# Optimization experiments

Hardware: AMD Instinct MI355X
Metric: run time of the kernel (lower is better)

The kernel has to match this reference:

```python
import jax, jax.numpy as jnp
import numpy as np

VOCAB = 50000
EMBED = 512
COMP = 300
B, L = 2048, 200
CENTER = jnp.array([40.7127, -74.0059], dtype=jnp.float32)


def setup_inputs() -> dict:
    key = jax.random.key(0)
    ks = jax.random.split(key, 8)
    words = jax.random.randint(ks[0], (B, L), 0, VOCAB, dtype=jnp.int64)
    features = jax.random.normal(ks[1], (B, 2), dtype=jnp.float32)
    mask = jnp.ones((B, L), dtype=jnp.float32)
    # nn.Linear(vocab_size, embedding_dim): weight [out, in]
    lim1 = 1.0 / np.sqrt(VOCAB)
    W_hidden = jax.random.uniform(ks[2], (EMBED, VOCAB), jnp.float32, -lim1, lim1)
    b_hidden = jax.random.uniform(ks[3], (EMBED,), jnp.float32, -lim1, lim1)
    lim2 = 1.0 / np.sqrt(EMBED)
    W_pi = jax.random.uniform(ks[4], (COMP, EMBED), jnp.float32, -lim2, lim2)
    b_pi = jax.random.uniform(ks[5], (COMP,), jnp.float32, -lim2, lim2)
    # mu = (rand-0.5)*4 + CENTER ; sigma = rand * log(0.01)
    mu = (jax.random.uniform(ks[6], (COMP, 2), jnp.float32) - 0.5) * 4.0 + CENTER
    sigma = jax.random.uniform(ks[7], (COMP, 2), jnp.float32) * np.log(0.01).astype(np.float32)
    return {"words": words, "features": features, "mask": mask,
            "W_hidden": W_hidden, "b_hidden": b_hidden,
            "W_pi": W_pi, "b_pi": b_pi, "mu": mu, "sigma": sigma}


def reference(words, features, mask, W_hidden, b_hidden, W_pi, b_pi, mu, sigma):
    bsz = words.shape[0]
    # binary bag-of-words one-hot: s[words[i]] = 1 (duplicates collapse to 1)
    q = jnp.zeros((bsz, VOCAB), dtype=W_hidden.dtype)
    q = q.at[jnp.arange(bsz)[:, None], words].set(1.0)
    hidden = jnp.tanh(q @ W_hidden.T + b_hidden)          # [B, E]
    pi = jax.nn.softmax(hidden @ W_pi.T + b_pi, axis=-1).T  # [C, B]
    sigma_out = jnp.exp(sigma)                             # [C, 2]
    return pi, sigma_out, mu
```

## Files before the change

kernel.cpp:

```cpp
#include <hip/hip_runtime.h>
#include <cstdint>
#include <cstddef>

#define VOCAB 50000
#define EMBED 512
#define COMP  300
#define LW    200
#define LPAD  208
#define NCHUNK 8
#define CHUNK_ROWS 50048
#define CHUNK_BYTES ((size_t)CHUNK_ROWS * 64)
#define CPAD  320

#define QINVSCALE 28398.0633f
#define QSCALE    3.52136689e-05f

__global__ __launch_bounds__(256) void quant_chunk_kernel(
    const float* __restrict__ in, unsigned char* __restrict__ out)
{
    __shared__ float tile[64 * 68];
    const int wBase = blockIdx.x * 64;
    const int c = blockIdx.y;
    const int eBase = c * 64;
    const int t = threadIdx.x;

    {
        const int col4 = t & 15;
        const int w = wBase + col4 * 4;
#pragma unroll
        for (int rr = 0; rr < 4; ++rr) {
            const int el = (t >> 4) + rr * 16;
            float4 v = make_float4(0.f, 0.f, 0.f, 0.f);
            if (w + 3 < VOCAB) {
                v = *(const float4*)&in[(size_t)(eBase + el) * VOCAB + w];
            } else {
                const float* row = &in[(size_t)(eBase + el) * VOCAB];
                v.x = (w + 0 < VOCAB) ? row[w + 0] : 0.f;
                v.y = (w + 1 < VOCAB) ? row[w + 1] : 0.f;
                v.z = (w + 2 < VOCAB) ? row[w + 2] : 0.f;
                v.w = (w + 3 < VOCAB) ? row[w + 3] : 0.f;
            }
            *(float4*)&tile[el * 68 + col4 * 4] = v;
        }
    }
    __syncthreads();

    {
        const int wl = t >> 2;
        const int g = t & 3;
        unsigned int pk[4];
#pragma unroll
        for (int q4 = 0; q4 < 4; ++q4) {
            unsigned int p = 0;
#pragma unroll
            for (int k = 0; k < 4; ++k) {
                const float f = tile[(g * 16 + q4 * 4 + k) * 68 + wl];
                int q = __float2int_rn(f * QINVSCALE) + 128;
                q = q < 0 ? 0 : (q > 255 ? 255 : q);
                p |= (unsigned int)q << (8 * k);
            }
            pk[q4] = p;
        }
        uint4 v = make_uint4(pk[0], pk[1], pk[2], pk[3]);
        *(uint4*)(out + (size_t)c * CHUNK_BYTES + (size_t)(wBase + wl) * 64 + g * 16) = v;
    }
}

__global__ __launch_bounds__(512) void wpi_tail_kernel(
    const float* __restrict__ W_pi, const float* __restrict__ mu,
    const float* __restrict__ sigma, float* __restrict__ Wtp,
    float* __restrict__ out_tail)
{
    const int c = blockIdx.x;
    const int k = threadIdx.x;
    Wtp[(size_t)k * CPAD + c] = (c < COMP) ? W_pi[(size_t)c * EMBED + k] : 0.f;
    if (c == 0) {
        for (int t = k; t < 2 * COMP; t += 512) {
            out_tail[t]            = expf(sigma[t]);
            out_tail[2 * COMP + t] = mu[t];
        }
    }
}

__global__ __launch_bounds__(256) void dedup_kernel(
    const int* __restrict__ words, int* __restrict__ soff)
{
    __shared__ int sw[LW];
    const int i = blockIdx.x;
    const int t = threadIdx.x;
    if (t < LW) sw[t] = words[(size_t)i * LW + t];
    __syncthreads();
    if (t < LPAD) {
        int off = VOCAB * 64;
        if (t < LW) {
            const int w = sw[t];
            int dup = 0;
            for (int j = 0; j < t; ++j) dup |= (sw[j] == w);
            off = (dup ? VOCAB : w) * 64;
        }
        soff[(size_t)i * LPAD + t] = off;
    }
}

__global__ __launch_bounds__(256) void gather_kernel(
    const int* __restrict__ soff, const unsigned char* __restrict__ W8,
    const float* __restrict__ b_hidden, float* __restrict__ hT, int B)
{
    __shared__ int sOff[LPAD];
    __shared__ float part[256];
    const int b = blockIdx.x;
    const int c = b & 7;
    const int i = b >> 3;
    const int t = threadIdx.x;
    const int w4 = t >> 6, lane = t & 63;

    if (t < LPAD) sOff[t] = soff[(size_t)i * LPAD + t];
    __syncthreads();

    const unsigned char* base = W8 + (size_t)c * CHUNK_BYTES + (lane & 15) * 4;
    const int j = lane >> 4;
    const int l0 = w4 * 52;
    float a0 = 0.f, a1 = 0.f, a2 = 0.f, a3 = 0.f;
#pragma unroll
    for (int s = 0; s < 13; ++s) {
        const int off = sOff[l0 + s * 4 + j];
        const unsigned int d = *(const unsigned int*)(base + (unsigned int)off);
        a0 += (float)(d & 0xffu);
        a1 += (float)((d >> 8) & 0xffu);
        a2 += (float)((d >> 16) & 0xffu);
        a3 += (float)(d >> 24);
    }
    a0 += __shfl_xor(a0, 16); a0 += __shfl_xor(a0, 32);
    a1 += __shfl_xor(a1, 16); a1 += __shfl_xor(a1, 32);
    a2 += __shfl_xor(a2, 16); a2 += __shfl_xor(a2, 32);
    a3 += __shfl_xor(a3, 16); a3 += __shfl_xor(a3, 32);
    if (lane < 16)
        *(float4*)&part[w4 * 64 + lane * 4] = make_float4(a0, a1, a2, a3);
    __syncthreads();

    if (t < 64) {
        const float S = part[t] + part[64 + t] + part[128 + t] + part[192 + t];
        const int e = c * 64 + t;
        hT[(size_t)e * B + i] = tanhf((S - 26624.0f) * QSCALE + b_hidden[e]);
    }
}

__global__ __launch_bounds__(256) void logits_kernel(
    const float* __restrict__ hT, const float* __restrict__ Wtp,
    const float* __restrict__ b_pi, float* __restrict__ logit, int B)
{
    __shared__ float sh[256 * 64];
    const int i0 = blockIdx.x * 64;
    const int cblk = blockIdx.y;
    const int t = threadIdx.x;
    const int wv = __builtin_amdgcn_readfirstlane(t >> 6);
    const int lane = t & 63;
    const int c0 = cblk * 32 + wv * 8;

    float acc[8] = {0.f, 0.f, 0.f, 0.f, 0.f, 0.f, 0.f, 0.f};

    for (int ks = 0; ks < EMBED; ks += 256) {
        __syncthreads();
#pragma unroll
        for (int p = 0; p < 16; ++p) {
            const int q = p * 256 + t;
            const int k = q >> 4;
            const int f4 = q & 15;
            *(float4*)&sh[k * 64 + f4 * 4] =
                *(const float4*)&hT[(size_t)(ks + k) * B + i0 + f4 * 4];
        }
        __syncthreads();

#pragma unroll 4
        for (int k = 0; k < 256; ++k) {
            const float h = sh[k * 64 + lane];
            const float* __restrict__ wrow = &Wtp[(size_t)(ks + k) * CPAD + c0];
#pragma unroll
            for (int jj = 0; jj < 8; ++jj)
                acc[jj] = fmaf(h, wrow[jj], acc[jj]);
        }
    }

#pragma unroll
    for (int jj = 0; jj < 8; ++jj) {
        const int cc = c0 + jj;
        if (cc < COMP)
            logit[(size_t)cc * B + i0 + lane] = acc[jj] + b_pi[cc];
    }
}

__global__ __launch_bounds__(64) void softmax_kernel(
    const float* __restrict__ logit, float* __restrict__ pi_out, int B)
{
    const int i = blockIdx.x * 64 + threadIdx.x;
    float m = -INFINITY, l = 0.f;
#pragma unroll 4
    for (int c = 0; c < COMP; ++c) {
        const float x = logit[(size_t)c * B + i];
        const float mn = fmaxf(m, x);
        l = l * __expf(m - mn) + __expf(x - mn);
        m = mn;
    }
    const float inv = 1.0f / l;
#pragma unroll 4
    for (int c = 0; c < COMP; ++c) {
        const float x = logit[(size_t)c * B + i];
        pi_out[(size_t)c * B + i] = __expf(x - m) * inv;
    }
}

extern "C" void kernel_launch(void* const* d_in, const int* in_sizes, int n_in,
                              void* d_out, int out_size, void* d_ws, size_t ws_size,
                              hipStream_t stream) {
    const int*   words    = (const int*)d_in[0];
    const float* W_hidden = (const float*)d_in[3];
    const float* b_hidden = (const float*)d_in[4];
    const float* W_pi     = (const float*)d_in[5];
    const float* b_pi     = (const float*)d_in[6];
    const float* mu       = (const float*)d_in[7];
    const float* sigma    = (const float*)d_in[8];
    float* out = (float*)d_out;

    const int B = in_sizes[0] / LW;

    unsigned char* W8   = (unsigned char*)d_ws;
    int*   soff  = (int*)(W8 + NCHUNK * CHUNK_BYTES);
    float* hT    = (float*)(soff + (size_t)B * LPAD);
    float* Wtp   = hT + (size_t)EMBED * B;
    float* logit = Wtp + (size_t)EMBED * CPAD;

    hipLaunchKernelGGL(quant_chunk_kernel, dim3(CHUNK_ROWS / 64, NCHUNK), dim3(256),
                       0, stream, W_hidden, W8);
    hipLaunchKernelGGL(wpi_tail_kernel, dim3(CPAD), dim3(512), 0, stream,
                       W_pi, mu, sigma, Wtp, out + (size_t)COMP * B);
    hipLaunchKernelGGL(dedup_kernel, dim3(B), dim3(256), 0, stream, words, soff);
    hipLaunchKernelGGL(gather_kernel, dim3(B * NCHUNK), dim3(256), 0, stream,
                       soff, W8, b_hidden, hT, B);
    hipLaunchKernelGGL(logits_kernel, dim3(B / 64, 10), dim3(256), 0, stream,
                       hT, Wtp, b_pi, logit, B);
    hipLaunchKernelGGL(softmax_kernel, dim3(B / 64), dim3(64), 0, stream,
                       logit, out, B);
}
```

Before: 290.6 us.

## Coalesce hidden and W_pi transposes, split softmax with partial max/sum

```diff
diff --git a/kernel.cpp b/kernel.cpp
--- a/kernel.cpp
+++ b/kernel.cpp
@@ -11,6 +11,7 @@
 #define CHUNK_ROWS 50048
 #define CHUNK_BYTES ((size_t)CHUNK_ROWS * 64)
 #define CPAD  320
+#define NPART 40
 
 #define QINVSCALE 28398.0633f
 #define QSCALE    3.52136689e-05f
@@ -66,18 +67,42 @@
     }
 }
 
-__global__ __launch_bounds__(512) void wpi_tail_kernel(
+__global__ __launch_bounds__(256) void wpi_tail_kernel(
     const float* __restrict__ W_pi, const float* __restrict__ mu,
     const float* __restrict__ sigma, float* __restrict__ Wtp,
     float* __restrict__ out_tail)
 {
-    const int c = blockIdx.x;
-    const int k = threadIdx.x;
-    Wtp[(size_t)k * CPAD + c] = (c < COMP) ? W_pi[(size_t)c * EMBED + k] : 0.f;
-    if (c == 0) {
-        for (int t = k; t < 2 * COMP; t += 512) {
-            out_tail[t]            = expf(sigma[t]);
-            out_tail[2 * COMP + t] = mu[t];
+    __shared__ float tile[32 * 33];
+    const int kBase = blockIdx.x * 32;
+    const int cBase = blockIdx.y * 32;
+    const int t = threadIdx.x;
+
+    {
+        const int cr = t >> 3;
+        const int k4 = t & 7;
+        float4 v = make_float4(0.f, 0.f, 0.f, 0.f);
+        if (cBase + cr < COMP)
+            v = *(const float4*)&W_pi[(size_t)(cBase + cr) * EMBED + kBase + k4 * 4];
+        tile[cr * 33 + k4 * 4 + 0] = v.x;
+        tile[cr * 33 + k4 * 4 + 1] = v.y;
+        tile[cr * 33 + k4 * 4 + 2] = v.z;
+        tile[cr * 33 + k4 * 4 + 3] = v.w;
+    }
+    __syncthreads();
+    {
+        const int kr = t >> 3;
+        const int c4 = t & 7;
+        float4 v;
+        v.x = tile[(c4 * 4 + 0) * 33 + kr];
+        v.y = tile[(c4 * 4 + 1) * 33 + kr];
+        v.z = tile[(c4 * 4 + 2) * 33 + kr];
+        v.w = tile[(c4 * 4 + 3) * 33 + kr];
+        *(float4*)&Wtp[(size_t)(kBase + kr) * CPAD + cBase + c4 * 4] = v;
+    }
+    if (blockIdx.x == 0 && blockIdx.y == 0) {
+        for (int tt = t; tt < 2 * COMP; tt += 256) {
+            out_tail[tt]            = expf(sigma[tt]);
+            out_tail[2 * COMP + tt] = mu[tt];
         }
     }
 }
@@ -104,7 +129,7 @@
 
 __global__ __launch_bounds__(256) void gather_kernel(
     const int* __restrict__ soff, const unsigned char* __restrict__ W8,
-    const float* __restrict__ b_hidden, float* __restrict__ hT, int B)
+    const float* __restrict__ b_hidden, float* __restrict__ h)
 {
     __shared__ int sOff[LPAD];
     __shared__ float part[256];
@@ -141,15 +166,48 @@
     if (t < 64) {
         const float S = part[t] + part[64 + t] + part[128 + t] + part[192 + t];
         const int e = c * 64 + t;
-        hT[(size_t)e * B + i] = tanhf((S - 26624.0f) * QSCALE + b_hidden[e]);
+        h[(size_t)i * EMBED + e] = tanhf((S - 26624.0f) * QSCALE + b_hidden[e]);
+    }
+}
+
+__global__ __launch_bounds__(256) void htrans_kernel(
+    const float* __restrict__ h, float* __restrict__ hT, int B)
+{
+    __shared__ float tile[64 * 65];
+    const int i0 = blockIdx.x * 64;
+    const int k0 = blockIdx.y * 64;
+    const int t = threadIdx.x;
+    const int col4 = t & 15;
+    const int row = t >> 4;
+
+#pragma unroll
+    for (int rr = 0; rr < 4; ++rr) {
+        const int r = row + rr * 16;
+        const float4 v = *(const float4*)&h[(size_t)(i0 + r) * EMBED + k0 + col4 * 4];
+        tile[r * 65 + col4 * 4 + 0] = v.x;
+        tile[r * 65 + col4 * 4 + 1] = v.y;
+        tile[r * 65 + col4 * 4 + 2] = v.z;
+        tile[r * 65 + col4 * 4 + 3] = v.w;
+    }
+    __syncthreads();
+#pragma unroll
+    for (int rr = 0; rr < 4; ++rr) {
+        const int kr = row + rr * 16;
+        float4 v;
+        v.x = tile[(col4 * 4 + 0) * 65 + kr];
+        v.y = tile[(col4 * 4 + 1) * 65 + kr];
+        v.z = tile[(col4 * 4 + 2) * 65 + kr];
+        v.w = tile[(col4 * 4 + 3) * 65 + kr];
+        *(float4*)&hT[(size_t)(k0 + kr) * B + i0 + col4 * 4] = v;
     }
 }
 
 __global__ __launch_bounds__(256) void logits_kernel(
     const float* __restrict__ hT, const float* __restrict__ Wtp,
-    const float* __restrict__ b_pi, float* __restrict__ logit, int B)
-{
-    __shared__ float sh[256 * 64];
+    const float* __restrict__ b_pi, float* __restrict__ logit,
+    float* __restrict__ pm, float* __restrict__ pl, int B)
+{
+    __shared__ float sh[128 * 64];
     const int i0 = blockIdx.x * 64;
     const int cblk = blockIdx.y;
     const int t = threadIdx.x;
@@ -159,10 +217,10 @@
 
     float acc[8] = {0.f, 0.f, 0.f, 0.f, 0.f, 0.f, 0.f, 0.f};
 
-    for (int ks = 0; ks < EMBED; ks += 256) {
+    for (int ks = 0; ks < EMBED; ks += 128) {
         __syncthreads();
 #pragma unroll
-        for (int p = 0; p < 16; ++p) {
+        for (int p = 0; p < 8; ++p) {
             const int q = p * 256 + t;
             const int k = q >> 4;
             const int f4 = q & 15;
@@ -172,40 +230,58 @@
         __syncthreads();
 
 #pragma unroll 4
-        for (int k = 0; k < 256; ++k) {
-            const float h = sh[k * 64 + lane];
+        for (int k = 0; k < 128; ++k) {
+            const float hh = sh[k * 64 + lane];
             const float* __restrict__ wrow = &Wtp[(size_t)(ks + k) * CPAD + c0];
 #pragma unroll
             for (int jj = 0; jj < 8; ++jj)
-                acc[jj] = fmaf(h, wrow[jj], acc[jj]);
-        }
-    }
-
+                acc[jj] = fmaf(hh, wrow[jj], acc[jj]);
+        }
+    }
+
+    float vals[8];
+    float m = -INFINITY;
 #pragma unroll
     for (int jj = 0; jj < 8; ++jj) {
         const int cc = c0 + jj;
-        if (cc < COMP)
-            logit[(size_t)cc * B + i0 + lane] = acc[jj] + b_pi[cc];
-    }
+        if (cc < COMP) {
+            const float v = acc[jj] + b_pi[cc];
+            vals[jj] = v;
+            logit[(size_t)cc * B + i0 + lane] = v;
+            m = fmaxf(m, v);
+        } else {
+            vals[jj] = -INFINITY;
+        }
+    }
+    float l = 0.f;
+#pragma unroll
+    for (int jj = 0; jj < 8; ++jj) {
+        if (c0 + jj < COMP) l += __expf(vals[jj] - m);
+    }
+    const int g = cblk * 4 + wv;
+    pm[(size_t)g * B + i0 + lane] = m;
+    pl[(size_t)g * B + i0 + lane] = l;
 }
 
 __global__ __launch_bounds__(64) void softmax_kernel(
-    const float* __restrict__ logit, float* __restrict__ pi_out, int B)
+    const float* __restrict__ logit, const float* __restrict__ pm,
+    const float* __restrict__ pl, float* __restrict__ pi_out, int B)
 {
     const int i = blockIdx.x * 64 + threadIdx.x;
-    float m = -INFINITY, l = 0.f;
-#pragma unroll 4
-    for (int c = 0; c < COMP; ++c) {
+    const int part = blockIdx.y;
+    float M = -INFINITY;
+#pragma unroll 8
+    for (int g = 0; g < NPART; ++g) M = fmaxf(M, pm[(size_t)g * B + i]);
+    float L = 0.f;
+#pragma unroll 8
+    for (int g = 0; g < NPART; ++g)
+        L += pl[(size_t)g * B + i] * __expf(pm[(size_t)g * B + i] - M);
+    const float inv = 1.0f / L;
+    const int cEnd = part * 75 + 75;
+#pragma unroll 5
+    for (int c = part * 75; c < cEnd; ++c) {
         const float x = logit[(size_t)c * B + i];
-        const float mn = fmaxf(m, x);
-        l = l * __expf(m - mn) + __expf(x - mn);
-        m = mn;
-    }
-    const float inv = 1.0f / l;
-#pragma unroll 4
-    for (int c = 0; c < COMP; ++c) {
-        const float x = logit[(size_t)c * B + i];
-        pi_out[(size_t)c * B + i] = __expf(x - m) * inv;
+        pi_out[(size_t)c * B + i] = __expf(x - M) * inv;
     }
 }
 
@@ -225,19 +301,24 @@
 
     unsigned char* W8   = (unsigned char*)d_ws;
     int*   soff  = (int*)(W8 + NCHUNK * CHUNK_BYTES);
-    float* hT    = (float*)(soff + (size_t)B * LPAD);
+    float* h     = (float*)(soff + (size_t)B * LPAD);
+    float* hT    = h  + (size_t)B * EMBED;
     float* Wtp   = hT + (size_t)EMBED * B;
     float* logit = Wtp + (size_t)EMBED * CPAD;
+    float* pm    = logit + (size_t)COMP * B;
+    float* pl    = pm + (size_t)NPART * B;
 
     hipLaunchKernelGGL(quant_chunk_kernel, dim3(CHUNK_ROWS / 64, NCHUNK), dim3(256),
                        0, stream, W_hidden, W8);
-    hipLaunchKernelGGL(wpi_tail_kernel, dim3(CPAD), dim3(512), 0, stream,
-                       W_pi, mu, sigma, Wtp, out + (size_t)COMP * B);
+    hipLaunchKernelGGL(wpi_tail_kernel, dim3(EMBED / 32, CPAD / 32), dim3(256),
+                       0, stream, W_pi, mu, sigma, Wtp, out + (size_t)COMP * B);
     hipLaunchKernelGGL(dedup_kernel, dim3(B), dim3(256), 0, stream, words, soff);
     hipLaunchKernelGGL(gather_kernel, dim3(B * NCHUNK), dim3(256), 0, stream,
-                       soff, W8, b_hidden, hT, B);
+                       soff, W8, b_hidden, h);
+    hipLaunchKernelGGL(htrans_kernel, dim3(B / 64, EMBED / 64), dim3(256),
+                       0, stream, h, hT, B);
     hipLaunchKernelGGL(logits_kernel, dim3(B / 64, 10), dim3(256), 0, stream,
-                       hT, Wtp, b_pi, logit, B);
-    hipLaunchKernelGGL(softmax_kernel, dim3(B / 64), dim3(64), 0, stream,
-                       logit, out, B);
-}
+                       hT, Wtp, b_pi, logit, pm, pl, B);
+    hipLaunchKernelGGL(softmax_kernel, dim3(B / 64, 4), dim3(64), 0, stream,
+                       logit, pm, pl, out, B);
+}
```

After: 262.0 us. -9.8%, faster.
